# Kernel optimization log

Hardware: AMD Instinct MI355X
Metric: run time of the kernel (lower is better)

The kernel has to match this reference:

```python
import jax, jax.numpy as jnp
import numpy as np

B, LS, VS = 4, 1024, 1024
VH, LH, H = 1024, 1024, 16
HD = LH // H  # head_dim = 64


def setup_inputs() -> dict:
    key = jax.random.key(0)
    ks = jax.random.split(key, 10)
    s = 0.02
    return {
        "v_hidden_states": jax.random.normal(ks[0], (B, VS, VH), jnp.float32),
        "l_hidden_states": jax.random.normal(ks[1], (B, LS, LH), jnp.float32),
        "q_w": jax.random.normal(ks[2], (LH, LH), jnp.float32) * s,
        "q_b": jnp.zeros((LH,), jnp.float32),
        "k_w": jax.random.normal(ks[3], (VH, LH), jnp.float32) * s,
        "k_b": jnp.zeros((LH,), jnp.float32),
        "v_w": jax.random.normal(ks[4], (VH, LH), jnp.float32) * s,
        "v_b": jnp.zeros((LH,), jnp.float32),
        "o_w": jax.random.normal(ks[5], (LH, LH), jnp.float32) * s,
        "o_b": jnp.zeros((LH,), jnp.float32),
    }


def reference(v_hidden_states, l_hidden_states, q_w, q_b, k_w, k_b, v_w, v_b, o_w, o_b):
    b, ls, _ = l_hidden_states.shape
    vs = v_hidden_states.shape[1]
    q = (l_hidden_states @ q_w + q_b).reshape(b, ls, H, HD)
    k = (v_hidden_states @ k_w + k_b).reshape(b, vs, H, HD)
    v = (v_hidden_states @ v_w + v_b).reshape(b, vs, H, HD)
    # NOTE: original scales by sqrt(hidden_size), not sqrt(head_dim)
    scale = jnp.sqrt(jnp.asarray(LH, q.dtype))
    scores = jnp.einsum("blhd,bvhd->bhlv", q, k) / scale
    attn = jax.nn.softmax(scores, axis=-1)
    out = jnp.einsum("bhlv,bvhd->blhd", attn, v).reshape(b, ls, LH)
    return out @ o_w + o_b
```

## Files before the change

### kernel.cpp

```cpp
#include <hip/hip_runtime.h>

typedef __bf16 bf16;
typedef __attribute__((ext_vector_type(4))) __bf16 bf16x4;
typedef __attribute__((ext_vector_type(8))) __bf16 bf16x8;
typedef __attribute__((ext_vector_type(4))) float f32x4;

static __device__ __forceinline__ f32x4 mfma_16x16x32(bf16x8 a, bf16x8 b, f32x4 c) {
    return __builtin_amdgcn_mfma_f32_16x16x32_bf16(a, b, c, 0, 0, 0);
}

static __device__ __forceinline__ bf16x8 load8(const float* p) {
    f32x4 a = *(const f32x4*)p;
    f32x4 b = *(const f32x4*)(p + 4);
    bf16x8 r;
    r[0] = (bf16)a[0]; r[1] = (bf16)a[1]; r[2] = (bf16)a[2]; r[3] = (bf16)a[3];
    r[4] = (bf16)b[0]; r[5] = (bf16)b[1]; r[6] = (bf16)b[2]; r[7] = (bf16)b[3];
    return r;
}

static __device__ __forceinline__ void gload_lds16(const void* g, void* l) {
    __builtin_amdgcn_global_load_lds(
        (const __attribute__((address_space(1))) void*)g,
        (__attribute__((address_space(3))) void*)l, 16, 0, 0);
}

#define QSCALE 0.0450842200277801f

__global__ __launch_bounds__(256) void prep_kernel(
    const float* __restrict__ l_h, const float* __restrict__ v_h,
    const float* __restrict__ w0, const float* __restrict__ w1,
    const float* __restrict__ w2, const float* __restrict__ w3,
    bf16* __restrict__ l_bf, bf16* __restrict__ v_bf,
    bf16* __restrict__ dq, bf16* __restrict__ dkv, bf16* __restrict__ dov)
{
    const int id = blockIdx.x;
    if (id < 4096) {
        const float* s = (id < 2048) ? l_h : v_h;
        bf16*       d = (id < 2048) ? l_bf : v_bf;
        const int   bb = (id < 2048) ? id : id - 2048;
        const size_t i = ((size_t)bb * 256 + threadIdx.x) * 8;
        *(bf16x8*)(d + i) = load8(s + i);
        return;
    }
    const int widx = id - 4096;
    const int z    = widx >> 8;
    const int rem  = widx & 255;
    const int j0   = (rem & 15) * 64;
    const int i0   = (rem >> 4) * 64;
    const float* src; bf16* dst;
    switch (z) {
        case 0:  src = w0; dst = dq; break;
        case 1:  src = w1; dst = dkv; break;
        case 2:  src = w2; dst = dkv + (size_t)1024 * 1024; break;
        default: src = w3; dst = dov; break;
    }
    const float wscale = (z == 0) ? QSCALE : 1.0f;
    __shared__ float T[64][65];
    const int tx = threadIdx.x & 15;
    const int ty = threadIdx.x >> 4;
    #pragma unroll
    for (int it = 0; it < 4; ++it) {
        f32x4 v = *(const f32x4*)(src + (size_t)(i0 + ty + it * 16) * 1024 + j0 + tx * 4);
        T[ty + it * 16][tx * 4 + 0] = v[0];
        T[ty + it * 16][tx * 4 + 1] = v[1];
        T[ty + it * 16][tx * 4 + 2] = v[2];
        T[ty + it * 16][tx * 4 + 3] = v[3];
    }
    __syncthreads();
    #pragma unroll
    for (int it = 0; it < 4; ++it) {
        const int jj = ty + it * 16;
        bf16x4 o;
        o[0] = (bf16)(T[tx * 4 + 0][jj] * wscale);
        o[1] = (bf16)(T[tx * 4 + 1][jj] * wscale);
        o[2] = (bf16)(T[tx * 4 + 2][jj] * wscale);
        o[3] = (bf16)(T[tx * 4 + 3][jj] * wscale);
        *(bf16x4*)(dst + (size_t)(j0 + jj) * 1024 + i0 + tx * 4) = o;
    }
}

__global__ __launch_bounds__(256, 3) void proj128_kernel(
    const bf16* __restrict__ l_bf, const bf16* __restrict__ v_bf,
    const bf16* __restrict__ QWt,  const bf16* __restrict__ KVWt,
    const float* __restrict__ q_b, const float* __restrict__ k_b,
    const float* __restrict__ v_b,
    bf16* __restrict__ Qh, bf16* __restrict__ Kh, bf16* __restrict__ Vt)
{
    __shared__ __align__(16) bf16 As[128][32];
    __shared__ __align__(16) bf16 Bs[128][32];

    const int t    = threadIdx.x;
    const int lane = t & 63;
    const int wave = t >> 6;
    const int wm   = wave & 1;
    const int wn   = wave >> 1;
    const int l15  = lane & 15;
    const int quad = lane >> 4;

    const bool isQ = blockIdx.x < 8;
    const bf16* A  = isQ ? l_bf : v_bf;
    const bf16* Bt = isQ ? QWt  : KVWt;
    const int  gn0 = (isQ ? blockIdx.x : blockIdx.x - 8) * 128;
    const int  gm0 = blockIdx.y * 128;
    const int  K   = 1024;

    const int srow    = lane >> 2;
    const int chunk_g = (lane & 3) ^ ((srow >> 1) & 3);
    const size_t aoff = (size_t)(gm0 + wave * 32 + srow) * K + chunk_g * 8;
    const size_t boff = (size_t)(gn0 + wave * 32 + srow) * K + chunk_g * 8;

    f32x4 acc[4][4];
    #pragma unroll
    for (int i = 0; i < 4; ++i)
        #pragma unroll
        for (int j = 0; j < 4; ++j)
            acc[i][j] = (f32x4){0.f, 0.f, 0.f, 0.f};

    for (int k0 = 0; k0 < K; k0 += 32) {
        #pragma unroll
        for (int q = 0; q < 2; ++q) {
            gload_lds16(A  + aoff + (size_t)q * 16 * K + k0, &As[wave * 32 + q * 16][0]);
            gload_lds16(Bt + boff + (size_t)q * 16 * K + k0, &Bs[wave * 32 + q * 16][0]);
        }
        __syncthreads();

        bf16x8 af[4], bfr[4];
        #pragma unroll
        for (int mt = 0; mt < 4; ++mt) {
            const int row = wm * 64 + mt * 16 + l15;
            af[mt] = *(const bf16x8*)(&As[row][(quad ^ ((row >> 1) & 3)) * 8]);
        }
        #pragma unroll
        for (int nt = 0; nt < 4; ++nt) {
            const int row = wn * 64 + nt * 16 + l15;
            bfr[nt] = *(const bf16x8*)(&Bs[row][(quad ^ ((row >> 1) & 3)) * 8]);
        }
        #pragma unroll
        for (int mt = 0; mt < 4; ++mt)
            #pragma unroll
            for (int nt = 0; nt < 4; ++nt)
                acc[mt][nt] = mfma_16x16x32(af[mt], bfr[nt], acc[mt][nt]);

        __syncthreads();
    }

    #pragma unroll
    for (int nt = 0; nt < 4; ++nt) {
        const int col = gn0 + wn * 64 + nt * 16 + l15;
        float bb; bf16* dst; bool hm;
        if (isQ)             { bb = q_b[col] * QSCALE;   dst = Qh; hm = true;  }
        else if (col < 1024) { bb = k_b[col];            dst = Kh; hm = true;  }
        else                 { bb = v_b[col - 1024];     dst = Vt; hm = false; }
        #pragma unroll
        for (int mt = 0; mt < 4; ++mt) {
            #pragma unroll
            for (int r = 0; r < 4; ++r) {
                const int row = gm0 + wm * 64 + mt * 16 + quad * 4 + r;
                const float v = acc[mt][nt][r] + bb;
                if (hm) {
                    const size_t idx =
                        ((size_t)((row >> 10) * 16 + (col >> 6)) * 1024 +
                         (row & 1023)) * 64 + (col & 63);
                    dst[idx] = (bf16)v;
                } else {
                    const int vc = col - 1024;
                    const size_t idx =
                        ((size_t)((row >> 10) * 16 + (vc >> 6)) * 64 +
                         (vc & 63)) * 1024 + (row & 1023);
                    dst[idx] = (bf16)v;
                }
            }
        }
    }
}

static __device__ __forceinline__ void gemm_core_128x64(
    const bf16* __restrict__ A, const bf16* __restrict__ Bt, int K,
    int gm0, int gn0, bf16 (*As)[32], bf16 (*Bs)[32], f32x4 acc[4][2])
{
    const int t    = threadIdx.x;
    const int lane = t & 63;
    const int wave = t >> 6;
    const int wm   = wave & 1;
    const int wn   = wave >> 1;
    const int l15  = lane & 15;
    const int quad = lane >> 4;

    const int srow    = lane >> 2;
    const int chunk_g = (lane & 3) ^ ((srow >> 1) & 3);
    const size_t aoff = (size_t)(gm0 + wave * 32 + srow) * K + chunk_g * 8;
    const size_t boff = (size_t)(gn0 + wave * 16 + srow) * K + chunk_g * 8;

    #pragma unroll
    for (int i = 0; i < 4; ++i)
        #pragma unroll
        for (int j = 0; j < 2; ++j)
            acc[i][j] = (f32x4){0.f, 0.f, 0.f, 0.f};

    for (int k0 = 0; k0 < K; k0 += 32) {
        gload_lds16(A + aoff + k0,                  &As[wave * 32][0]);
        gload_lds16(A + aoff + (size_t)16 * K + k0, &As[wave * 32 + 16][0]);
        gload_lds16(Bt + boff + k0,                 &Bs[wave * 16][0]);
        __syncthreads();

        bf16x8 af[4], bfr[2];
        #pragma unroll
        for (int mt = 0; mt < 4; ++mt) {
            const int row = wm * 64 + mt * 16 + l15;
            af[mt] = *(const bf16x8*)(&As[row][(quad ^ ((row >> 1) & 3)) * 8]);
        }
        #pragma unroll
        for (int nt = 0; nt < 2; ++nt) {
            const int row = wn * 32 + nt * 16 + l15;
            bfr[nt] = *(const bf16x8*)(&Bs[row][(quad ^ ((row >> 1) & 3)) * 8]);
        }
        #pragma unroll
        for (int mt = 0; mt < 4; ++mt)
            #pragma unroll
            for (int nt = 0; nt < 2; ++nt)
                acc[mt][nt] = mfma_16x16x32(af[mt], bfr[nt], acc[mt][nt]);

        __syncthreads();
    }
}

__global__ __launch_bounds__(256, 3) void ogemm_kernel(
    const bf16* __restrict__ Aw, const bf16* __restrict__ OWt,
    const float* __restrict__ o_b, float* __restrict__ C)
{
    __shared__ __align__(16) bf16 As[128][32];
    __shared__ __align__(16) bf16 Bs[64][32];

    const int gn0 = blockIdx.x * 64;
    const int gm0 = blockIdx.y * 128;

    f32x4 acc[4][2];
    gemm_core_128x64(Aw, OWt, 1024, gm0, gn0, As, Bs, acc);

    const int lane = threadIdx.x & 63;
    const int wave = threadIdx.x >> 6;
    const int wm   = wave & 1;
    const int wn   = wave >> 1;
    const int l15  = lane & 15;
    const int quad = lane >> 4;

    #pragma unroll
    for (int nt = 0; nt < 2; ++nt) {
        const int col = gn0 + wn * 32 + nt * 16 + l15;
        const float bb = o_b[col];
        #pragma unroll
        for (int mt = 0; mt < 4; ++mt) {
            #pragma unroll
            for (int r = 0; r < 4; ++r) {
                const int row = gm0 + wm * 64 + mt * 16 + quad * 4 + r;
                C[(size_t)row * 1024 + col] = acc[mt][nt][r] + bb;
            }
        }
    }
}

__global__ __launch_bounds__(256) void attn_kernel(
    const bf16* __restrict__ Q, const bf16* __restrict__ K,
    const bf16* __restrict__ V, bf16* __restrict__ O)
{
    const int t    = threadIdx.x;
    const int lane = t & 63;
    const int wave = t >> 6;
    const int l15  = lane & 15;
    const int quad = lane >> 4;

    const int head = blockIdx.x;
    const int q0   = blockIdx.y * 128;
    const int b    = head >> 4;
    const int h    = head & 15;

    __shared__ __align__(16) bf16 Kb[2][64][64];
    __shared__ __align__(16) bf16 Vb[2][64][64];
    __shared__ __align__(16) bf16 P[4][32][72];

    const bf16* Qp  = Q + ((size_t)head * 1024 + q0 + wave * 32) * 64;
    const bf16* Kp  = K + (size_t)head * 1024 * 64;
    const bf16* Vtp = V + (size_t)head * 64 * 1024;

    const int r8  = lane >> 3;
    const int c8  = lane & 7;
    const int swz = (c8 ^ r8) * 8;

    bf16x8 aq[2][2];
    #pragma unroll
    for (int mt = 0; mt < 2; ++mt)
        #pragma unroll
        for (int kc = 0; kc < 2; ++kc)
            aq[mt][kc] = *(const bf16x8*)(Qp + (mt * 16 + l15) * 64 + kc * 32 + quad * 8);

    bf16x8 vones;
    #pragma unroll
    for (int j = 0; j < 8; ++j) vones[j] = (bf16)1.0f;

    f32x4 oacc[2][4];
    #pragma unroll
    for (int mt = 0; mt < 2; ++mt)
        #pragma unroll
        for (int nt = 0; nt < 4; ++nt)
            oacc[mt][nt] = (f32x4){0.f, 0.f, 0.f, 0.f};
    f32x4 lacc[2];
    lacc[0] = (f32x4){0.f, 0.f, 0.f, 0.f};
    lacc[1] = (f32x4){0.f, 0.f, 0.f, 0.f};

    #define STAGE(c, buf)                                                          \
        {                                                                          \
            const int kv0_ = (c) * 64;                                             \
            _Pragma("unroll")                                                      \
            for (int g = 0; g < 2; ++g) {                                          \
                const int R = wave * 16 + g * 8;                                   \
                gload_lds16(Kp + (size_t)(kv0_ + R + r8) * 64 + swz,               \
                            &Kb[buf][R][0]);                                       \
                gload_lds16(Vtp + (size_t)(R + r8) * 1024 + kv0_ + swz,            \
                            &Vb[buf][R][0]);                                       \
            }                                                                      \
        }

    STAGE(0, 0);

    const int sw = l15 & 7;

    for (int c = 0; c < 16; ++c) {
        const int buf = c & 1;
        __syncthreads();
        if (c + 1 < 16) STAGE(c + 1, buf ^ 1);

        #pragma unroll
        for (int nt = 0; nt < 4; ++nt) {
            const bf16* krow = &Kb[buf][nt * 16 + l15][0];
            bf16x8 bk0 = *(const bf16x8*)(krow + (quad ^ sw) * 8);
            bf16x8 bk1 = *(const bf16x8*)(krow + ((quad + 4) ^ sw) * 8);
            #pragma unroll
            for (int mt = 0; mt < 2; ++mt) {
                f32x4 s = (f32x4){0.f, 0.f, 0.f, 0.f};
                s = mfma_16x16x32(aq[mt][0], bk0, s);
                s = mfma_16x16x32(aq[mt][1], bk1, s);
                #pragma unroll
                for (int r = 0; r < 4; ++r) {
                    const float e = __builtin_amdgcn_exp2f(s[r]);
                    P[wave][mt * 16 + quad * 4 + r][nt * 16 + l15] = (bf16)e;
                }
            }
        }

        #pragma unroll
        for (int mt = 0; mt < 2; ++mt) {
            bf16x8 pa0 = *(const bf16x8*)(&P[wave][mt * 16 + l15][quad * 8]);
            bf16x8 pa1 = *(const bf16x8*)(&P[wave][mt * 16 + l15][32 + quad * 8]);
            lacc[mt] = mfma_16x16x32(pa0, vones, lacc[mt]);
            lacc[mt] = mfma_16x16x32(pa1, vones, lacc[mt]);
            #pragma unroll
            for (int nt = 0; nt < 4; ++nt) {
                const bf16* vrow = &Vb[buf][nt * 16 + l15][0];
                bf16x8 bv0 = *(const bf16x8*)(vrow + (quad ^ sw) * 8);
                bf16x8 bv1 = *(const bf16x8*)(vrow + ((quad + 4) ^ sw) * 8);
                oacc[mt][nt] = mfma_16x16x32(pa0, bv0, oacc[mt][nt]);
                oacc[mt][nt] = mfma_16x16x32(pa1, bv1, oacc[mt][nt]);
            }
        }
    }
    #undef STAGE

    #pragma unroll
    for (int mt = 0; mt < 2; ++mt) {
        const float invs[4] = {1.0f / lacc[mt][0], 1.0f / lacc[mt][1],
                               1.0f / lacc[mt][2], 1.0f / lacc[mt][3]};
        #pragma unroll
        for (int nt = 0; nt < 4; ++nt) {
            #pragma unroll
            for (int r = 0; r < 4; ++r) {
                const int row = q0 + wave * 32 + mt * 16 + quad * 4 + r;
                O[((size_t)b * 1024 + row) * 1024 + h * 64 + nt * 16 + l15] =
                    (bf16)(oacc[mt][nt][r] * invs[r]);
            }
        }
    }
}

extern "C" void kernel_launch(void* const* d_in, const int* in_sizes, int n_in,
                              void* d_out, int out_size, void* d_ws, size_t ws_size,
                              hipStream_t stream)
{
    const float* v_h = (const float*)d_in[0];
    const float* l_h = (const float*)d_in[1];
    const float* q_w = (const float*)d_in[2];
    const float* q_b = (const float*)d_in[3];
    const float* k_w = (const float*)d_in[4];
    const float* k_b = (const float*)d_in[5];
    const float* v_w = (const float*)d_in[6];
    const float* v_b = (const float*)d_in[7];
    const float* o_w = (const float*)d_in[8];
    const float* o_b = (const float*)d_in[9];
    float* out = (float*)d_out;

    const size_t SZ = (size_t)4096 * 1024;
    const size_t WZ = (size_t)1024 * 1024;

    bf16* l_bf = (bf16*)d_ws;
    bf16* v_bf = l_bf + SZ;
    bf16* QWt  = v_bf + SZ;
    bf16* KVWt = QWt + WZ;
    bf16* OWt  = KVWt + 2 * WZ;
    bf16* Qh   = OWt + WZ;
    bf16* Kh   = Qh + SZ;
    bf16* Vt   = Kh + SZ;
    bf16* Aw   = Vt + SZ;

    prep_kernel<<<dim3(5120), 256, 0, stream>>>(
        l_h, v_h, q_w, k_w, v_w, o_w, l_bf, v_bf, QWt, KVWt, OWt);

    proj128_kernel<<<dim3(24, 32), 256, 0, stream>>>(
        l_bf, v_bf, QWt, KVWt, q_b, k_b, v_b, Qh, Kh, Vt);

    attn_kernel<<<dim3(64, 8), 256, 0, stream>>>(Qh, Kh, Vt, Aw);

    ogemm_kernel<<<dim3(16, 32), 256, 0, stream>>>(Aw, OWt, o_b, out);

    (void)in_sizes; (void)n_in; (void)out_size; (void)ws_size;
}
```

Before: 192.7 us.

## Double-buffer LDS tiles in projection and output GEMM kernels

```diff
diff --git a/kernel.cpp b/kernel.cpp
--- a/kernel.cpp
+++ b/kernel.cpp
@@ -86,8 +86,8 @@
     const float* __restrict__ v_b,
     bf16* __restrict__ Qh, bf16* __restrict__ Kh, bf16* __restrict__ Vt)
 {
-    __shared__ __align__(16) bf16 As[128][32];
-    __shared__ __align__(16) bf16 Bs[128][32];
+    __shared__ __align__(16) bf16 As[2][128][32];
+    __shared__ __align__(16) bf16 Bs[2][128][32];
 
     const int t    = threadIdx.x;
     const int lane = t & 63;
@@ -116,24 +116,34 @@
         for (int j = 0; j < 4; ++j)
             acc[i][j] = (f32x4){0.f, 0.f, 0.f, 0.f};
 
+    #define PSTAGE(k0_, buf_)                                                      \
+        {                                                                          \
+            _Pragma("unroll")                                                      \
+            for (int q = 0; q < 2; ++q) {                                          \
+                gload_lds16(A  + aoff + (size_t)q * 16 * K + (k0_),                \
+                            &As[buf_][wave * 32 + q * 16][0]);                     \
+                gload_lds16(Bt + boff + (size_t)q * 16 * K + (k0_),                \
+                            &Bs[buf_][wave * 32 + q * 16][0]);                     \
+            }                                                                      \
+        }
+
+    PSTAGE(0, 0);
+    __syncthreads();
+
     for (int k0 = 0; k0 < K; k0 += 32) {
-        #pragma unroll
-        for (int q = 0; q < 2; ++q) {
-            gload_lds16(A  + aoff + (size_t)q * 16 * K + k0, &As[wave * 32 + q * 16][0]);
-            gload_lds16(Bt + boff + (size_t)q * 16 * K + k0, &Bs[wave * 32 + q * 16][0]);
-        }
-        __syncthreads();
+        const int buf = (k0 >> 5) & 1;
+        if (k0 + 32 < K) PSTAGE(k0 + 32, buf ^ 1);
 
         bf16x8 af[4], bfr[4];
         #pragma unroll
         for (int mt = 0; mt < 4; ++mt) {
             const int row = wm * 64 + mt * 16 + l15;
-            af[mt] = *(const bf16x8*)(&As[row][(quad ^ ((row >> 1) & 3)) * 8]);
+            af[mt] = *(const bf16x8*)(&As[buf][row][(quad ^ ((row >> 1) & 3)) * 8]);
         }
         #pragma unroll
         for (int nt = 0; nt < 4; ++nt) {
             const int row = wn * 64 + nt * 16 + l15;
-            bfr[nt] = *(const bf16x8*)(&Bs[row][(quad ^ ((row >> 1) & 3)) * 8]);
+            bfr[nt] = *(const bf16x8*)(&Bs[buf][row][(quad ^ ((row >> 1) & 3)) * 8]);
         }
         #pragma unroll
         for (int mt = 0; mt < 4; ++mt)
@@ -143,6 +153,7 @@
 
         __syncthreads();
     }
+    #undef PSTAGE
 
     #pragma unroll
     for (int nt = 0; nt < 4; ++nt) {
@@ -176,7 +187,7 @@
 
 static __device__ __forceinline__ void gemm_core_128x64(
     const bf16* __restrict__ A, const bf16* __restrict__ Bt, int K,
-    int gm0, int gn0, bf16 (*As)[32], bf16 (*Bs)[32], f32x4 acc[4][2])
+    int gm0, int gn0, bf16 (*As)[128][32], bf16 (*Bs)[64][32], f32x4 acc[4][2])
 {
     const int t    = threadIdx.x;
     const int lane = t & 63;
@@ -197,22 +208,30 @@
         for (int j = 0; j < 2; ++j)
             acc[i][j] = (f32x4){0.f, 0.f, 0.f, 0.f};
 
+    #define OSTAGE(k0_, buf_)                                                     \
+        {                                                                         \
+            gload_lds16(A + aoff + (k0_),                  &As[buf_][wave * 32][0]);       \
+            gload_lds16(A + aoff + (size_t)16 * K + (k0_), &As[buf_][wave * 32 + 16][0]);  \
+            gload_lds16(Bt + boff + (k0_),                 &Bs[buf_][wave * 16][0]);       \
+        }
+
+    OSTAGE(0, 0);
+    __syncthreads();
+
     for (int k0 = 0; k0 < K; k0 += 32) {
-        gload_lds16(A + aoff + k0,                  &As[wave * 32][0]);
-        gload_lds16(A + aoff + (size_t)16 * K + k0, &As[wave * 32 + 16][0]);
-        gload_lds16(Bt + boff + k0,                 &Bs[wave * 16][0]);
-        __syncthreads();
+        const int buf = (k0 >> 5) & 1;
+        if (k0 + 32 < K) OSTAGE(k0 + 32, buf ^ 1);
 
         bf16x8 af[4], bfr[2];
         #pragma unroll
         for (int mt = 0; mt < 4; ++mt) {
             const int row = wm * 64 + mt * 16 + l15;
-            af[mt] = *(const bf16x8*)(&As[row][(quad ^ ((row >> 1) & 3)) * 8]);
+            af[mt] = *(const bf16x8*)(&As[buf][row][(quad ^ ((row >> 1) & 3)) * 8]);
         }
         #pragma unroll
         for (int nt = 0; nt < 2; ++nt) {
             const int row = wn * 32 + nt * 16 + l15;
-            bfr[nt] = *(const bf16x8*)(&Bs[row][(quad ^ ((row >> 1) & 3)) * 8]);
+            bfr[nt] = *(const bf16x8*)(&Bs[buf][row][(quad ^ ((row >> 1) & 3)) * 8]);
         }
         #pragma unroll
         for (int mt = 0; mt < 4; ++mt)
@@ -222,14 +241,15 @@
 
         __syncthreads();
     }
+    #undef OSTAGE
 }
 
 __global__ __launch_bounds__(256, 3) void ogemm_kernel(
     const bf16* __restrict__ Aw, const bf16* __restrict__ OWt,
     const float* __restrict__ o_b, float* __restrict__ C)
 {
-    __shared__ __align__(16) bf16 As[128][32];
-    __shared__ __align__(16) bf16 Bs[64][32];
+    __shared__ __align__(16) bf16 As[2][128][32];
+    __shared__ __align__(16) bf16 Bs[2][64][32];
 
     const int gn0 = blockIdx.x * 64;
     const int gm0 = blockIdx.y * 128;
```

Measured after the change: 200.7 us. +4.2%, slower.
